# Optimization experiments

Measured on AMD Instinct MI355X. Metric: run time of the kernel, lower is better.

The kernel has to match this reference:

```python
import jax, jax.numpy as jnp
import numpy as np

NUM_EMBEDDINGS = 1024
EMBEDDING_DIM = 256
N_TOKENS = 65536


def setup_inputs() -> dict:
    key = jax.random.key(0)
    k1, k2 = jax.random.split(key)
    z_e = jax.random.normal(k1, (N_TOKENS, EMBEDDING_DIM), dtype=jnp.float32)
    # codebook init: uniform(-1/K, 1/K) as in torch Embedding init override
    codebook = jax.random.uniform(
        k2, (NUM_EMBEDDINGS, EMBEDDING_DIM), dtype=jnp.float32,
        minval=-1.0 / NUM_EMBEDDINGS, maxval=1.0 / NUM_EMBEDDINGS)
    return {"z_e": z_e, "codebook": codebook}


def reference(z_e, codebook):
    x_norm2 = jnp.sum(z_e * z_e, axis=1, keepdims=True)            # [N,1]
    c_norm2 = jnp.sum(codebook * codebook, axis=1)[None, :]         # [1,K]
    dist = x_norm2 + c_norm2 - 2.0 * (z_e @ codebook.T)             # [N,K]
    nearest = jnp.argmin(dist, axis=1)                               # [N]
    z_q = codebook[nearest]                                          # [N,D]

    # MSE with reduction='sum'
    embedding_loss = jnp.sum((jax.lax.stop_gradient(z_e) - z_q) ** 2)
    commitment_loss = jnp.sum((z_e - jax.lax.stop_gradient(z_q)) ** 2)
    vq_loss = embedding_loss + commitment_loss

    # straight-through estimator
    z_q_out = z_e + jax.lax.stop_gradient(z_q - z_e)
    return z_q_out, vq_loss
```

## Files before the change

kernel.cpp:

```cpp
#include <hip/hip_runtime.h>
#include <float.h>
#include <stdint.h>

#define N_TOKENS 65536
#define N_EMB    1024
#define DIM      256

typedef __attribute__((ext_vector_type(4))) float f32x4;

template <bool HI>
__device__ __forceinline__ unsigned pk8(float a, float b, unsigned old) {
    return (unsigned)__builtin_amdgcn_cvt_pk_fp8_f32(a, b, (int)old, HI);
}

__device__ __forceinline__ void gld_lds16(const void* g, void* l) {
    __builtin_amdgcn_global_load_lds(
        (__attribute__((address_space(1))) void*)(g),
        (__attribute__((address_space(3))) void*)(l), 16, 0, 0);
}

__global__ __launch_bounds__(256) void prep_kernel(const float* __restrict__ cb,
                                                   float* __restrict__ cn2,
                                                   unsigned char* __restrict__ img) {
    const int t = threadIdx.x, w = t >> 6, lane = t & 63;
#pragma unroll
    for (int u = 0; u < 2; ++u) {
        const int c = blockIdx.x * 8 + w * 2 + u;
        float4 v = ((const float4*)cb)[c * 64 + lane];
        float s = v.x * v.x + v.y * v.y + v.z * v.z + v.w * v.w;
#pragma unroll
        for (int m = 1; m < 64; m <<= 1) s += __shfl_xor(s, m);
        if (lane == 0) cn2[c] = s;
        unsigned pw = pk8<false>(512.f * v.x, 512.f * v.y, 0);
        pw = pk8<true>(512.f * v.z, 512.f * v.w, pw);
        const int sp = (lane & 15) >> 2, q = lane & 3;
        unsigned u0 = (unsigned)__shfl((int)pw, sp * 16 + q * 2);
        unsigned u1 = (unsigned)__shfl((int)pw, sp * 16 + q * 2 + 1);
        unsigned u2 = (unsigned)__shfl((int)pw, sp * 16 + 8 + q * 2);
        unsigned u3 = (unsigned)__shfl((int)pw, sp * 16 + 8 + q * 2 + 1);
        if (lane < 16) {
            int T = c >> 5, ph = sp * 2 + ((c >> 4) & 1);
            int gid = T * 512 + ph * 64 + q * 16 + (c & 15);
            uint4 o; o.x = u0; o.y = u1; o.z = u2; o.w = u3;
            ((uint4*)img)[gid] = o;
        }
    }
}

__global__ __launch_bounds__(256, 4) void fused_vq_kernel(
        const float* __restrict__ z, const unsigned char* __restrict__ cbimg,
        const float* __restrict__ cb, const float* __restrict__ cn2,
        float* __restrict__ out, float* __restrict__ partials) {
    __shared__ char  Bs[3][8192];
    __shared__ float cnS[N_EMB];
    __shared__ int   winS[64];
    __shared__ float distS[64];
    __shared__ float xnS[64];
    const int t = threadIdx.x;
    const int lane = t & 63, w = t >> 6;
    const int col = lane & 15, g = lane >> 4;

    const char* srcL = (const char*)cbimg + w * 2048 + lane * 16;
    char* q0 = &Bs[0][0] + w * 2048;
    char* q1 = &Bs[1][0] + w * 2048;
    char* q2 = &Bs[2][0] + w * 2048;

    gld_lds16(srcL,        q0);
    gld_lds16(srcL + 1024, q0 + 1024);
    gld_lds16(srcL + 8192,        q1);
    gld_lds16(srcL + 8192 + 1024, q1 + 1024);

    long  ah[8];
    float xnp = 0.f;
    const int row = blockIdx.x * 64 + w * 16 + col;
#pragma unroll
    for (int s = 0; s < 8; ++s) {
        const float* p = z + (size_t)row * DIM + s * 32 + g * 8;
        float4 x0 = *(const float4*)p;
        float4 x1 = *(const float4*)(p + 4);
        xnp = fmaf(x0.x, x0.x, xnp); xnp = fmaf(x0.y, x0.y, xnp);
        xnp = fmaf(x0.z, x0.z, xnp); xnp = fmaf(x0.w, x0.w, xnp);
        xnp = fmaf(x1.x, x1.x, xnp); xnp = fmaf(x1.y, x1.y, xnp);
        xnp = fmaf(x1.z, x1.z, xnp); xnp = fmaf(x1.w, x1.w, xnp);
        unsigned w0, w1;
        w0 = pk8<false>(-64.f * x0.x, -64.f * x0.y, 0);
        w0 = pk8<true> (-64.f * x0.z, -64.f * x0.w, w0);
        w1 = pk8<false>(-64.f * x1.x, -64.f * x1.y, 0);
        w1 = pk8<true> (-64.f * x1.z, -64.f * x1.w, w1);
        ah[s] = (long)((((unsigned long long)w1) << 32) | w0);
    }
    xnp += __shfl_xor(xnp, 16);
    xnp += __shfl_xor(xnp, 32);
    if (g == 0) xnS[w * 16 + col] = xnp;
#pragma unroll
    for (int i = 0; i < 4; ++i) cnS[t + i * 256] = cn2[t + i * 256];

    float best[4];
    int   bidx[4];
#pragma unroll
    for (int r = 0; r < 4; ++r) { best[r] = FLT_MAX; bidx[r] = 0; }

    asm volatile("s_waitcnt lgkmcnt(0)" ::: "memory");

    const char* rd0 = &Bs[0][0];
    const char* rd1 = &Bs[1][0];
    const char* rd2 = &Bs[2][0];
    char *wq0 = q0, *wq1 = q1, *wq2 = q2;

    for (int T = 0; T < 32; ++T) {
        if (T < 31) asm volatile("s_waitcnt vmcnt(2)" ::: "memory");
        else        asm volatile("s_waitcnt vmcnt(0)" ::: "memory");
        __builtin_amdgcn_s_barrier();
        __builtin_amdgcn_sched_barrier(0);
        if (T + 2 < 32) {
            const char* s2 = srcL + (T + 2) * 8192;
            gld_lds16(s2,        wq2);
            gld_lds16(s2 + 1024, wq2 + 1024);
        }
        const f32x4 zero4 = {0.f, 0.f, 0.f, 0.f};
        f32x4 a0 = zero4, a1 = zero4;
        __builtin_amdgcn_s_setprio(1);
#pragma unroll
        for (int sp = 0; sp < 4; ++sp) {
            long2 b0 = *(const long2*)(rd0 + (sp * 2 + 0) * 1024 + (lane << 4));
            long2 b1 = *(const long2*)(rd0 + (sp * 2 + 1) * 1024 + (lane << 4));
            a0 = __builtin_amdgcn_mfma_f32_16x16x32_fp8_fp8(ah[2*sp],   b0.x, a0, 0, 0, 0);
            a0 = __builtin_amdgcn_mfma_f32_16x16x32_fp8_fp8(ah[2*sp+1], b0.y, a0, 0, 0, 0);
            a1 = __builtin_amdgcn_mfma_f32_16x16x32_fp8_fp8(ah[2*sp],   b1.x, a1, 0, 0, 0);
            a1 = __builtin_amdgcn_mfma_f32_16x16x32_fp8_fp8(ah[2*sp+1], b1.y, a1, 0, 0, 0);
        }
        __builtin_amdgcn_s_setprio(0);
        {
            int   code0 = T * 32 + col;
            float cn0 = cnS[code0];
            int   code1 = code0 + 16;
            float cn1 = cnS[code1];
#pragma unroll
            for (int r = 0; r < 4; ++r) {
                float s0 = fmaf(a0[r], 6.103515625e-05f, cn0);
                if (s0 < best[r]) { best[r] = s0; bidx[r] = code0; }
                float s1 = fmaf(a1[r], 6.103515625e-05f, cn1);
                if (s1 < best[r]) { best[r] = s1; bidx[r] = code1; }
            }
        }
        const char* tr = rd0; rd0 = rd1; rd1 = rd2; rd2 = tr;
        char* tw = wq0; wq0 = wq1; wq1 = wq2; wq2 = tw;
    }

#pragma unroll
    for (int r = 0; r < 4; ++r) {
        float sc = best[r];
        int   cd = bidx[r];
#pragma unroll
        for (int mask = 1; mask <= 8; mask <<= 1) {
            float os = __shfl_xor(sc, mask);
            int   oc = __shfl_xor(cd, mask);
            if (os < sc || (os == sc && oc < cd)) { sc = os; cd = oc; }
        }
        if (col == 0) {
            int tl = w * 16 + g * 4 + r;
            winS[tl]  = cd;
            distS[tl] = sc;
        }
    }
    __syncthreads();

    if (t < 64) {
        float s = xnS[t] + distS[t];
#pragma unroll
        for (int m = 1; m < 64; m <<= 1) s += __shfl_xor(s, m);
        if (t == 0) partials[blockIdx.x] = s;
    }
    const size_t ob = (size_t)blockIdx.x * 4096;
#pragma unroll 4
    for (int i = 0; i < 16; ++i) {
        int f = i * 256 + t;
        int tl = f >> 6, c4 = f & 63;
        float4 qv = ((const float4*)cb)[winS[tl] * 64 + c4];
        ((float4*)out)[ob + f] = qv;
    }
}

__global__ __launch_bounds__(256) void reduce_kernel(const float* __restrict__ partials,
                                                     float* __restrict__ out_loss) {
    const int tid = threadIdx.x;
    float s = 0.f;
#pragma unroll
    for (int u = 0; u < 4; ++u) s += partials[tid + 256 * u];
#pragma unroll
    for (int m = 1; m < 64; m <<= 1) s += __shfl_xor(s, m);
    __shared__ float wsum[4];
    if ((tid & 63) == 0) wsum[tid >> 6] = s;
    __syncthreads();
    if (tid == 0) *out_loss = 2.0f * ((wsum[0] + wsum[1]) + (wsum[2] + wsum[3]));
}

extern "C" void kernel_launch(void* const* d_in, const int* in_sizes, int n_in,
                              void* d_out, int out_size, void* d_ws, size_t ws_size,
                              hipStream_t stream) {
    const float* z  = (const float*)d_in[0];
    const float* cb = (const float*)d_in[1];
    float* out = (float*)d_out;
    char*  ws  = (char*)d_ws;

    float*         cn2      = (float*)(ws);
    float*         partials = (float*)(ws + 4096);
    unsigned char* cbimg    = (unsigned char*)(ws + 8192);

    prep_kernel    <<<128, 256, 0, stream>>>(cb, cn2, cbimg);
    fused_vq_kernel<<<1024, 256, 0, stream>>>(z, cbimg, cb, cn2, out, partials);
    reduce_kernel  <<<1, 256, 0, stream>>>(partials, out + (size_t)N_TOKENS * DIM);
}
```

Measured before the change: 53.76 us.

## Switch distance GEMM to int8 MFMA with 128-row blocks and integer argmax

Quantizes tokens and codebook to int8 and replaces the fp8 16x16x32 MFMAs with int8 16x16x64 MFMAs. The codebook norm is folded into the integer accumulator init, so the argmin becomes an integer max compare. Each block now covers 128 tokens as two M tiles that share every codebook tile loaded into LDS, halving the grid and cutting codebook traffic per token. The exchange is much coarser quantization (tokens truncated with x*16, codebook clamped to ±127), which may change which code wins, plus fewer resident blocks per CU under the new launch bound.

```diff
diff --git a/kernel.cpp b/kernel.cpp
--- a/kernel.cpp
+++ b/kernel.cpp
@@ -6,12 +6,7 @@
 #define N_EMB    1024
 #define DIM      256
 
-typedef __attribute__((ext_vector_type(4))) float f32x4;
-
-template <bool HI>
-__device__ __forceinline__ unsigned pk8(float a, float b, unsigned old) {
-    return (unsigned)__builtin_amdgcn_cvt_pk_fp8_f32(a, b, (int)old, HI);
-}
+typedef __attribute__((ext_vector_type(4))) int int4v;
 
 __device__ __forceinline__ void gld_lds16(const void* g, void* l) {
     __builtin_amdgcn_global_load_lds(
@@ -21,6 +16,7 @@
 
 __global__ __launch_bounds__(256) void prep_kernel(const float* __restrict__ cb,
                                                    float* __restrict__ cn2,
+                                                   int* __restrict__ cnI,
                                                    unsigned char* __restrict__ img) {
     const int t = threadIdx.x, w = t >> 6, lane = t & 63;
 #pragma unroll
@@ -30,32 +26,38 @@
         float s = v.x * v.x + v.y * v.y + v.z * v.z + v.w * v.w;
 #pragma unroll
         for (int m = 1; m < 64; m <<= 1) s += __shfl_xor(s, m);
-        if (lane == 0) cn2[c] = s;
-        unsigned pw = pk8<false>(512.f * v.x, 512.f * v.y, 0);
-        pw = pk8<true>(512.f * v.z, 512.f * v.w, pw);
-        const int sp = (lane & 15) >> 2, q = lane & 3;
-        unsigned u0 = (unsigned)__shfl((int)pw, sp * 16 + q * 2);
-        unsigned u1 = (unsigned)__shfl((int)pw, sp * 16 + q * 2 + 1);
-        unsigned u2 = (unsigned)__shfl((int)pw, sp * 16 + 8 + q * 2);
-        unsigned u3 = (unsigned)__shfl((int)pw, sp * 16 + 8 + q * 2 + 1);
+        if (lane == 0) { cn2[c] = s; cnI[c] = (int)rintf(s * 1048576.f); }
+        int a0 = (int)fminf(fmaxf(rintf(v.x * 131072.f), -127.f), 127.f);
+        int a1 = (int)fminf(fmaxf(rintf(v.y * 131072.f), -127.f), 127.f);
+        int a2 = (int)fminf(fmaxf(rintf(v.z * 131072.f), -127.f), 127.f);
+        int a3 = (int)fminf(fmaxf(rintf(v.w * 131072.f), -127.f), 127.f);
+        unsigned pw = (a0 & 255) | ((a1 & 255) << 8) | ((a2 & 255) << 16) | ((a3 & 255) << 24);
+        int src = (lane >> 2) * 16 + (lane & 3) * 4;
+        unsigned u0 = (unsigned)__shfl((int)pw, src + 0);
+        unsigned u1 = (unsigned)__shfl((int)pw, src + 1);
+        unsigned u2 = (unsigned)__shfl((int)pw, src + 2);
+        unsigned u3 = (unsigned)__shfl((int)pw, src + 3);
         if (lane < 16) {
-            int T = c >> 5, ph = sp * 2 + ((c >> 4) & 1);
-            int gid = T * 512 + ph * 64 + q * 16 + (c & 15);
+            int ks = lane >> 2, g = lane & 3;
+            int T = c >> 5, half = (c >> 4) & 1;
+            int gid = T * 512 + (ks * 2 + half) * 64 + g * 16 + (c & 15);
             uint4 o; o.x = u0; o.y = u1; o.z = u2; o.w = u3;
             ((uint4*)img)[gid] = o;
         }
     }
 }
 
-__global__ __launch_bounds__(256, 4) void fused_vq_kernel(
+__global__ __launch_bounds__(256, 2) void fused_vq_kernel(
         const float* __restrict__ z, const unsigned char* __restrict__ cbimg,
         const float* __restrict__ cb, const float* __restrict__ cn2,
+        const int* __restrict__ cnI,
         float* __restrict__ out, float* __restrict__ partials) {
     __shared__ char  Bs[3][8192];
     __shared__ float cnS[N_EMB];
-    __shared__ int   winS[64];
-    __shared__ float distS[64];
-    __shared__ float xnS[64];
+    __shared__ int   cnIS[N_EMB];
+    __shared__ int   winS[128];
+    __shared__ float distS[128];
+    __shared__ float xnS[128];
     const int t = threadIdx.x;
     const int lane = t & 63, w = t >> 6;
     const int col = lane & 15, g = lane >> 4;
@@ -70,35 +72,51 @@
     gld_lds16(srcL + 8192,        q1);
     gld_lds16(srcL + 8192 + 1024, q1 + 1024);
 
-    long  ah[8];
-    float xnp = 0.f;
-    const int row = blockIdx.x * 64 + w * 16 + col;
-#pragma unroll
-    for (int s = 0; s < 8; ++s) {
-        const float* p = z + (size_t)row * DIM + s * 32 + g * 8;
-        float4 x0 = *(const float4*)p;
-        float4 x1 = *(const float4*)(p + 4);
-        xnp = fmaf(x0.x, x0.x, xnp); xnp = fmaf(x0.y, x0.y, xnp);
-        xnp = fmaf(x0.z, x0.z, xnp); xnp = fmaf(x0.w, x0.w, xnp);
-        xnp = fmaf(x1.x, x1.x, xnp); xnp = fmaf(x1.y, x1.y, xnp);
-        xnp = fmaf(x1.z, x1.z, xnp); xnp = fmaf(x1.w, x1.w, xnp);
-        unsigned w0, w1;
-        w0 = pk8<false>(-64.f * x0.x, -64.f * x0.y, 0);
-        w0 = pk8<true> (-64.f * x0.z, -64.f * x0.w, w0);
-        w1 = pk8<false>(-64.f * x1.x, -64.f * x1.y, 0);
-        w1 = pk8<true> (-64.f * x1.z, -64.f * x1.w, w1);
-        ah[s] = (long)((((unsigned long long)w1) << 32) | w0);
-    }
-    xnp += __shfl_xor(xnp, 16);
-    xnp += __shfl_xor(xnp, 32);
-    if (g == 0) xnS[w * 16 + col] = xnp;
-#pragma unroll
-    for (int i = 0; i < 4; ++i) cnS[t + i * 256] = cn2[t + i * 256];
-
-    float best[4];
-    int   bidx[4];
-#pragma unroll
-    for (int r = 0; r < 4; ++r) { best[r] = FLT_MAX; bidx[r] = 0; }
+    int4v ah[2][4];
+    float xnp[2] = {0.f, 0.f};
+    const int rbase = blockIdx.x * 128 + w * 32 + col;
+#pragma unroll
+    for (int m = 0; m < 2; ++m) {
+#pragma unroll
+        for (int ks = 0; ks < 4; ++ks) {
+            const float* p = z + (size_t)(rbase + m * 16) * DIM + ks * 64 + g * 16;
+            float4 x0 = *(const float4*)p;
+            float4 x1 = *(const float4*)(p + 4);
+            float4 x2 = *(const float4*)(p + 8);
+            float4 x3 = *(const float4*)(p + 12);
+            xnp[m] = fmaf(x0.x, x0.x, xnp[m]); xnp[m] = fmaf(x0.y, x0.y, xnp[m]);
+            xnp[m] = fmaf(x0.z, x0.z, xnp[m]); xnp[m] = fmaf(x0.w, x0.w, xnp[m]);
+            xnp[m] = fmaf(x1.x, x1.x, xnp[m]); xnp[m] = fmaf(x1.y, x1.y, xnp[m]);
+            xnp[m] = fmaf(x1.z, x1.z, xnp[m]); xnp[m] = fmaf(x1.w, x1.w, xnp[m]);
+            xnp[m] = fmaf(x2.x, x2.x, xnp[m]); xnp[m] = fmaf(x2.y, x2.y, xnp[m]);
+            xnp[m] = fmaf(x2.z, x2.z, xnp[m]); xnp[m] = fmaf(x2.w, x2.w, xnp[m]);
+            xnp[m] = fmaf(x3.x, x3.x, xnp[m]); xnp[m] = fmaf(x3.y, x3.y, xnp[m]);
+            xnp[m] = fmaf(x3.z, x3.z, xnp[m]); xnp[m] = fmaf(x3.w, x3.w, xnp[m]);
+            int4v fr;
+#pragma unroll
+            for (int q = 0; q < 4; ++q) {
+                const float4& xq = q == 0 ? x0 : (q == 1 ? x1 : (q == 2 ? x2 : x3));
+                int b0 = (int)(xq.x * 16.f), b1 = (int)(xq.y * 16.f);
+                int b2 = (int)(xq.z * 16.f), b3 = (int)(xq.w * 16.f);
+                fr[q] = (b0 & 255) | ((b1 & 255) << 8) | ((b2 & 255) << 16) | ((b3 & 255) << 24);
+            }
+            ah[m][ks] = fr;
+        }
+    }
+    xnp[0] += __shfl_xor(xnp[0], 16); xnp[0] += __shfl_xor(xnp[0], 32);
+    xnp[1] += __shfl_xor(xnp[1], 16); xnp[1] += __shfl_xor(xnp[1], 32);
+    if (g == 0) { xnS[w * 32 + col] = xnp[0]; xnS[w * 32 + 16 + col] = xnp[1]; }
+#pragma unroll
+    for (int i = 0; i < 4; ++i) {
+        cnS[t + i * 256]  = cn2[t + i * 256];
+        cnIS[t + i * 256] = cnI[t + i * 256];
+    }
+
+    int best[2][4], bidx[2][4];
+#pragma unroll
+    for (int m = 0; m < 2; ++m)
+#pragma unroll
+        for (int r = 0; r < 4; ++r) { best[m][r] = INT32_MIN; bidx[m][r] = 0; }
 
     asm volatile("s_waitcnt lgkmcnt(0)" ::: "memory");
 
@@ -117,63 +135,63 @@
             gld_lds16(s2,        wq2);
             gld_lds16(s2 + 1024, wq2 + 1024);
         }
-        const f32x4 zero4 = {0.f, 0.f, 0.f, 0.f};
-        f32x4 a0 = zero4, a1 = zero4;
+        const int code0 = T * 32 + col;
+        const int code1 = code0 + 16;
+        const int c0I = cnIS[code0], c1I = cnIS[code1];
+        int4v a00 = {-c0I, -c0I, -c0I, -c0I};
+        int4v a01 = {-c1I, -c1I, -c1I, -c1I};
+        int4v a10 = a00, a11 = a01;
         __builtin_amdgcn_s_setprio(1);
 #pragma unroll
-        for (int sp = 0; sp < 4; ++sp) {
-            long2 b0 = *(const long2*)(rd0 + (sp * 2 + 0) * 1024 + (lane << 4));
-            long2 b1 = *(const long2*)(rd0 + (sp * 2 + 1) * 1024 + (lane << 4));
-            a0 = __builtin_amdgcn_mfma_f32_16x16x32_fp8_fp8(ah[2*sp],   b0.x, a0, 0, 0, 0);
-            a0 = __builtin_amdgcn_mfma_f32_16x16x32_fp8_fp8(ah[2*sp+1], b0.y, a0, 0, 0, 0);
-            a1 = __builtin_amdgcn_mfma_f32_16x16x32_fp8_fp8(ah[2*sp],   b1.x, a1, 0, 0, 0);
-            a1 = __builtin_amdgcn_mfma_f32_16x16x32_fp8_fp8(ah[2*sp+1], b1.y, a1, 0, 0, 0);
+        for (int ks = 0; ks < 4; ++ks) {
+            int4v b0 = *(const int4v*)(rd0 + (ks * 2 + 0) * 1024 + (lane << 4));
+            int4v b1 = *(const int4v*)(rd0 + (ks * 2 + 1) * 1024 + (lane << 4));
+            a00 = __builtin_amdgcn_mfma_i32_16x16x64_i8(ah[0][ks], b0, a00, 0, 0, 0);
+            a10 = __builtin_amdgcn_mfma_i32_16x16x64_i8(ah[1][ks], b0, a10, 0, 0, 0);
+            a01 = __builtin_amdgcn_mfma_i32_16x16x64_i8(ah[0][ks], b1, a01, 0, 0, 0);
+            a11 = __builtin_amdgcn_mfma_i32_16x16x64_i8(ah[1][ks], b1, a11, 0, 0, 0);
         }
         __builtin_amdgcn_s_setprio(0);
-        {
-            int   code0 = T * 32 + col;
-            float cn0 = cnS[code0];
-            int   code1 = code0 + 16;
-            float cn1 = cnS[code1];
-#pragma unroll
-            for (int r = 0; r < 4; ++r) {
-                float s0 = fmaf(a0[r], 6.103515625e-05f, cn0);
-                if (s0 < best[r]) { best[r] = s0; bidx[r] = code0; }
-                float s1 = fmaf(a1[r], 6.103515625e-05f, cn1);
-                if (s1 < best[r]) { best[r] = s1; bidx[r] = code1; }
-            }
+#pragma unroll
+        for (int r = 0; r < 4; ++r) {
+            if (a00[r] > best[0][r]) { best[0][r] = a00[r]; bidx[0][r] = code0; }
+            if (a01[r] > best[0][r]) { best[0][r] = a01[r]; bidx[0][r] = code1; }
+            if (a10[r] > best[1][r]) { best[1][r] = a10[r]; bidx[1][r] = code0; }
+            if (a11[r] > best[1][r]) { best[1][r] = a11[r]; bidx[1][r] = code1; }
         }
         const char* tr = rd0; rd0 = rd1; rd1 = rd2; rd2 = tr;
         char* tw = wq0; wq0 = wq1; wq1 = wq2; wq2 = tw;
     }
 
 #pragma unroll
-    for (int r = 0; r < 4; ++r) {
-        float sc = best[r];
-        int   cd = bidx[r];
-#pragma unroll
-        for (int mask = 1; mask <= 8; mask <<= 1) {
-            float os = __shfl_xor(sc, mask);
-            int   oc = __shfl_xor(cd, mask);
-            if (os < sc || (os == sc && oc < cd)) { sc = os; cd = oc; }
-        }
-        if (col == 0) {
-            int tl = w * 16 + g * 4 + r;
-            winS[tl]  = cd;
-            distS[tl] = sc;
-        }
-    }
+    for (int m = 0; m < 2; ++m)
+#pragma unroll
+        for (int r = 0; r < 4; ++r) {
+            int a  = best[m][r];
+            int cd = bidx[m][r];
+#pragma unroll
+            for (int mask = 1; mask <= 8; mask <<= 1) {
+                int oa = __shfl_xor(a, mask);
+                int oc = __shfl_xor(cd, mask);
+                if (oa > a || (oa == a && oc < cd)) { a = oa; cd = oc; }
+            }
+            if (col == 0) {
+                int tl = w * 32 + m * 16 + g * 4 + r;
+                winS[tl] = cd;
+                distS[tl] = fmaf((float)(a + cnIS[cd]), -9.5367431640625e-07f, cnS[cd]);
+            }
+        }
     __syncthreads();
 
     if (t < 64) {
-        float s = xnS[t] + distS[t];
+        float s = (xnS[t] + distS[t]) + (xnS[t + 64] + distS[t + 64]);
 #pragma unroll
         for (int m = 1; m < 64; m <<= 1) s += __shfl_xor(s, m);
         if (t == 0) partials[blockIdx.x] = s;
     }
-    const size_t ob = (size_t)blockIdx.x * 4096;
+    const size_t ob = (size_t)blockIdx.x * 8192;
 #pragma unroll 4
-    for (int i = 0; i < 16; ++i) {
+    for (int i = 0; i < 32; ++i) {
         int f = i * 256 + t;
         int tl = f >> 6, c4 = f & 63;
         float4 qv = ((const float4*)cb)[winS[tl] * 64 + c4];
@@ -184,9 +202,7 @@
 __global__ __launch_bounds__(256) void reduce_kernel(const float* __restrict__ partials,
                                                      float* __restrict__ out_loss) {
     const int tid = threadIdx.x;
-    float s = 0.f;
-#pragma unroll
-    for (int u = 0; u < 4; ++u) s += partials[tid + 256 * u];
+    float s = partials[tid] + partials[tid + 256];
 #pragma unroll
     for (int m = 1; m < 64; m <<= 1) s += __shfl_xor(s, m);
     __shared__ float wsum[4];
@@ -204,10 +220,11 @@
     char*  ws  = (char*)d_ws;
 
     float*         cn2      = (float*)(ws);
-    float*         partials = (float*)(ws + 4096);
-    unsigned char* cbimg    = (unsigned char*)(ws + 8192);
-
-    prep_kernel    <<<128, 256, 0, stream>>>(cb, cn2, cbimg);
-    fused_vq_kernel<<<1024, 256, 0, stream>>>(z, cbimg, cb, cn2, out, partials);
+    int*           cnI      = (int*)(ws + 4096);
+    float*         partials = (float*)(ws + 8192);
+    unsigned char* cbimg    = (unsigned char*)(ws + 16384);
+
+    prep_kernel    <<<128, 256, 0, stream>>>(cb, cn2, cnI, cbimg);
+    fused_vq_kernel<<<512, 256, 0, stream>>>(z, cbimg, cb, cn2, cnI, out, partials);
     reduce_kernel  <<<1, 256, 0, stream>>>(partials, out + (size_t)N_TOKENS * DIM);
 }
```

Result: faster. 50.81 us (-5.5%).
